# Kernel optimization log

Measured on AMD Instinct MI355X. Metric: run time of the kernel, lower is better.

The kernel has to match this reference:

```python
import jax, jax.numpy as jnp
import numpy as np

B, C2D, C3D, NC = 8, 256, 512, 128
H = W = 64
T = H3 = W3 = 16


def setup_inputs() -> dict:
    key = jax.random.key(0)
    ks = jax.random.split(key, 12)
    s = 0.02
    return {
        "features_2d": jax.random.normal(ks[0], (B, C2D, H, W), jnp.float32),
        "features_3d": jax.random.normal(ks[1], (B, C3D, T, H3, W3), jnp.float32),
        "Wq": jax.random.normal(ks[2], (NC, C2D), jnp.float32) * s,
        "bq": jax.random.normal(ks[3], (NC,), jnp.float32) * s,
        "Wk": jax.random.normal(ks[4], (NC, C3D), jnp.float32) * s,
        "bk": jax.random.normal(ks[5], (NC,), jnp.float32) * s,
        "Wv": jax.random.normal(ks[6], (NC, C3D), jnp.float32) * s,
        "bv": jax.random.normal(ks[7], (NC,), jnp.float32) * s,
        "Wo": jax.random.normal(ks[8], (C2D, NC), jnp.float32) * s,
        "bo": jax.random.normal(ks[9], (C2D,), jnp.float32) * s,
        "Wps": jax.random.normal(ks[10], (C2D, C2D, 3, 3), jnp.float32) * s,
        "bps": jax.random.normal(ks[11], (C2D,), jnp.float32) * s,
    }


def reference(features_2d, features_3d, Wq, bq, Wk, bk, Wv, bv, Wo, bo, Wps, bps):
    # 1x1 conv Q over 2D features: [B, NC, H*W] -> [B, N2d, NC]
    Q = jnp.einsum("bchw,oc->bohw", features_2d, Wq) + bq[None, :, None, None]
    Q = Q.reshape(B, NC, H * W).transpose(0, 2, 1)          # [B, N2d, NC]
    # 1x1 conv K/V over 3D features (no pooling: H3 <= max_height_3d)
    K = jnp.einsum("bcthw,oc->bothw", features_3d, Wk) + bk[None, :, None, None, None]
    V = jnp.einsum("bcthw,oc->bothw", features_3d, Wv) + bv[None, :, None, None, None]
    K = K.reshape(B, NC, T * H3 * W3)                        # [B, NC, N3d]
    V = V.reshape(B, NC, T * H3 * W3).transpose(0, 2, 1)     # [B, N3d, NC]
    # full non-local attention (no 1/sqrt(d) scaling, matching the torch code)
    att = jnp.einsum("bnc,bcm->bnm", Q, K)                   # [B, N2d, N3d]
    att = jax.nn.softmax(att, axis=-1)
    out = jnp.einsum("bnm,bmc->bnc", att, V)                 # [B, N2d, NC]
    out = out.transpose(0, 2, 1).reshape(B, NC, H, W)
    # 1x1 output conv back to channels_2d
    out = jnp.einsum("bchw,oc->bohw", out, Wo) + bo[None, :, None, None]
    # residual add + 3x3 post-sum conv
    x = features_2d + out
    y = jax.lax.conv_general_dilated(
        x, Wps, window_strides=(1, 1), padding="SAME",
        dimension_numbers=("NCHW", "OIHW", "NCHW"))
    return y + bps[None, :, None, None]
```

## Files before the change

kernel.cpp:

```cpp
#include <hip/hip_runtime.h>
#include <cstdint>

#define NB  8
#define C2  256
#define C3  512
#define NCH 128
#define NN2 4096
#define NN3 4096

using f4 = float4;
typedef float f32x16 __attribute__((ext_vector_type(16)));
typedef __bf16 bf16x8 __attribute__((ext_vector_type(8)));

union FragU {
    uint4    q;
    uint32_t u[4];
    bf16x8   v;
};

__device__ __forceinline__ unsigned short f2bf(float f) {
    uint32_t u = __float_as_uint(f);
    u += 0x7fffu + ((u >> 16) & 1u);
    return (unsigned short)(u >> 16);
}
__device__ __forceinline__ float bf2f(unsigned short h) {
    return __uint_as_float(((uint32_t)h) << 16);
}
__device__ __forceinline__ uint32_t pkbf(float lo, float hi) {
    union { __bf16 h[2]; uint32_t u; } t;
    t.h[0] = (__bf16)lo;
    t.h[1] = (__bf16)hi;
    return t.u;
}
__device__ __forceinline__ void fma4(float* acc, float a, const f4 w) {
    acc[0] = fmaf(a, w.x, acc[0]);
    acc[1] = fmaf(a, w.y, acc[1]);
    acc[2] = fmaf(a, w.z, acc[2]);
    acc[3] = fmaf(a, w.w, acc[3]);
}

__global__ __launch_bounds__(256) void wprep(const float* __restrict__ Wps,
                                             unsigned short* __restrict__ Wb) {
    int idx = blockIdx.x * 256 + threadIdx.x;
    int t = idx >> 16;
    int r = idx & 65535;
    int co = r >> 8, ci = r & 255;
    Wb[idx] = f2bf(Wps[((size_t)(co * 256 + ci)) * 9 + t]);
}

__global__ __launch_bounds__(256) void wprep2(const float* __restrict__ Wq,
                                              const float* __restrict__ Wk,
                                              const float* __restrict__ Wv,
                                              unsigned short* __restrict__ Wqb,
                                              unsigned short* __restrict__ Wkb,
                                              unsigned short* __restrict__ Wvb) {
    int idx = blockIdx.x * 256 + threadIdx.x;
    if (idx < 32768)        Wqb[idx]          = f2bf(Wq[idx]);
    else if (idx < 98304)   Wkb[idx - 32768]  = f2bf(Wk[idx - 32768]);
    else                    Wvb[idx - 98304]  = f2bf(Wv[idx - 98304]);
}

__global__ __launch_bounds__(256) void proj_q(const float* __restrict__ f2d,
                                              const unsigned short* __restrict__ Wqb,
                                              const float* __restrict__ bq,
                                              unsigned short* __restrict__ Q) {
    __shared__ __align__(16) unsigned short Xs[2][128 * 40];
    const int tid = threadIdx.x;
    const int b  = blockIdx.x >> 5;
    const int n0 = (blockIdx.x & 31) << 7;
    const int wn = tid >> 6;
    const int lane = tid & 63;
    const int i31 = lane & 31;
    const int h   = lane >> 5;
    const int kp = tid >> 4;
    const int nc = tid & 15;

    f32x16 aQ[4];
#pragma unroll
    for (int cf = 0; cf < 4; cf++)
#pragma unroll
        for (int r = 0; r < 16; r++) aQ[cf][r] = 0.f;

    float xlo[8], xhi[8];
    auto LOADC = [&](int k0) {
        const float* r0 = f2d + ((size_t)b * C2 + k0 + 2 * kp) * NN2 + n0 + nc;
        const float* r1 = r0 + NN2;
#pragma unroll
        for (int i = 0; i < 8; i++) { xlo[i] = r0[16 * i]; xhi[i] = r1[16 * i]; }
    };
    auto WRITEC = [&](int bi) {
        unsigned short* X = Xs[bi];
#pragma unroll
        for (int i = 0; i < 8; i++)
            *(uint32_t*)&X[(nc + 16 * i) * 40 + 2 * kp] = pkbf(xlo[i], xhi[i]);
    };

    LOADC(0); WRITEC(0); __syncthreads();
    int cur = 0;
    for (int c = 0; c < 8; c++) {
        if (c + 1 < 8) LOADC((c + 1) * 32);
        const int k0 = c * 32;
        FragU xf[2];
        xf[0].q = *(const uint4*)&Xs[cur][(wn * 32 + i31) * 40 + h * 8];
        xf[1].q = *(const uint4*)&Xs[cur][(wn * 32 + i31) * 40 + 16 + h * 8];
#pragma unroll
        for (int ks = 0; ks < 2; ks++) {
            const int ko = k0 + ks * 16 + h * 8;
#pragma unroll
            for (int cf = 0; cf < 4; cf++) {
                FragU wq;
                wq.q = *(const uint4*)&Wqb[(size_t)(cf * 32 + i31) * 256 + ko];
                aQ[cf] = __builtin_amdgcn_mfma_f32_32x32x16_bf16(wq.v, xf[ks].v, aQ[cf], 0, 0, 0);
            }
        }
        if (c + 1 < 8) WRITEC(cur ^ 1);
        __syncthreads();
        cur ^= 1;
    }
    const int nQ = n0 + wn * 32 + i31;
    unsigned short* Qrow = Q + ((size_t)b * NN2 + nQ) * NCH;
#pragma unroll
    for (int cf = 0; cf < 4; cf++)
#pragma unroll
        for (int tq = 0; tq < 4; tq++) {
            int c0 = cf * 32 + 8 * tq + 4 * h;
            f4 bb = *(const f4*)(bq + c0);
            ushort4 s;
            s.x = f2bf(aQ[cf][4 * tq + 0] + bb.x);
            s.y = f2bf(aQ[cf][4 * tq + 1] + bb.y);
            s.z = f2bf(aQ[cf][4 * tq + 2] + bb.z);
            s.w = f2bf(aQ[cf][4 * tq + 3] + bb.w);
            *(ushort4*)(Qrow + c0) = s;
        }
}

__global__ __launch_bounds__(256) void proj_kv(const float* __restrict__ f3d,
                                               const unsigned short* __restrict__ Wkb,
                                               const float* __restrict__ bk,
                                               const unsigned short* __restrict__ Wvb,
                                               const float* __restrict__ bv,
                                               unsigned short* __restrict__ K,
                                               unsigned short* __restrict__ Vt) {
    __shared__ __align__(16) unsigned short Xs[2][128 * 40];
    const int tid = threadIdx.x;
    const int b  = blockIdx.x >> 5;
    const int n0 = (blockIdx.x & 31) << 7;
    const int wn = tid >> 6;
    const int lane = tid & 63;
    const int i31 = lane & 31;
    const int h   = lane >> 5;
    const int kp = tid >> 4;
    const int nc = tid & 15;

    f32x16 aK[4], aV[4];
#pragma unroll
    for (int cf = 0; cf < 4; cf++)
#pragma unroll
        for (int r = 0; r < 16; r++) { aK[cf][r] = 0.f; aV[cf][r] = 0.f; }

    float xlo[8], xhi[8];
    auto LOADC = [&](int k0) {
        const float* r0 = f3d + ((size_t)b * C3 + k0 + 2 * kp) * NN3 + n0 + nc;
        const float* r1 = r0 + NN3;
#pragma unroll
        for (int i = 0; i < 8; i++) { xlo[i] = r0[16 * i]; xhi[i] = r1[16 * i]; }
    };
    auto WRITEC = [&](int bi) {
        unsigned short* X = Xs[bi];
#pragma unroll
        for (int i = 0; i < 8; i++)
            *(uint32_t*)&X[(nc + 16 * i) * 40 + 2 * kp] = pkbf(xlo[i], xhi[i]);
    };

    LOADC(0); WRITEC(0); __syncthreads();
    int cur = 0;
    for (int c = 0; c < 16; c++) {
        if (c + 1 < 16) LOADC((c + 1) * 32);
        const int k0 = c * 32;
        FragU xf[2];
        xf[0].q = *(const uint4*)&Xs[cur][(wn * 32 + i31) * 40 + h * 8];
        xf[1].q = *(const uint4*)&Xs[cur][(wn * 32 + i31) * 40 + 16 + h * 8];
#pragma unroll
        for (int ks = 0; ks < 2; ks++) {
            const int ko = k0 + ks * 16 + h * 8;
#pragma unroll
            for (int cf = 0; cf < 4; cf++) {
                FragU wk, wv;
                wk.q = *(const uint4*)&Wkb[(size_t)(cf * 32 + i31) * 512 + ko];
                wv.q = *(const uint4*)&Wvb[(size_t)(cf * 32 + i31) * 512 + ko];
                aK[cf] = __builtin_amdgcn_mfma_f32_32x32x16_bf16(wk.v, xf[ks].v, aK[cf], 0, 0, 0);
                aV[cf] = __builtin_amdgcn_mfma_f32_32x32x16_bf16(xf[ks].v, wv.v, aV[cf], 0, 0, 0);
            }
        }
        if (c + 1 < 16) WRITEC(cur ^ 1);
        __syncthreads();
        cur ^= 1;
    }
    const int nK = n0 + wn * 32 + i31;
    unsigned short* Krow = K + ((size_t)b * NN3 + nK) * NCH;
#pragma unroll
    for (int cf = 0; cf < 4; cf++)
#pragma unroll
        for (int tq = 0; tq < 4; tq++) {
            int c0 = cf * 32 + 8 * tq + 4 * h;
            f4 bb = *(const f4*)(bk + c0);
            ushort4 s;
            s.x = f2bf(aK[cf][4 * tq + 0] + bb.x);
            s.y = f2bf(aK[cf][4 * tq + 1] + bb.y);
            s.z = f2bf(aK[cf][4 * tq + 2] + bb.z);
            s.w = f2bf(aK[cf][4 * tq + 3] + bb.w);
            *(ushort4*)(Krow + c0) = s;
        }
#pragma unroll
    for (int cf = 0; cf < 4; cf++) {
        const int cV = cf * 32 + i31;
        const float bvv = bv[cV];
        unsigned short* Vrow = Vt + ((size_t)b * NCH + cV) * NN3;
#pragma unroll
        for (int tq = 0; tq < 4; tq++) {
            int nq = n0 + wn * 32 + 8 * tq + 4 * h;
            ushort4 s;
            s.x = f2bf(aV[cf][4 * tq + 0] + bvv);
            s.y = f2bf(aV[cf][4 * tq + 1] + bvv);
            s.z = f2bf(aV[cf][4 * tq + 2] + bvv);
            s.w = f2bf(aV[cf][4 * tq + 3] + bvv);
            *(ushort4*)(Vrow + nq) = s;
        }
    }
}

__global__ __launch_bounds__(256) void attn(const unsigned short* __restrict__ Qg,
                                            const unsigned short* __restrict__ Kg,
                                            const unsigned short* __restrict__ Vtg,
                                            unsigned short* __restrict__ AO) {
    __shared__ __align__(16) unsigned short smem[32768];
    const int tid = threadIdx.x;
    const int b  = blockIdx.x >> 6;
    const int qc = blockIdx.x & 63;
    const int wid = tid >> 6;
    const int lane = tid & 63;
    const int i31 = lane & 31;
    const int h   = lane >> 5;
    const int p    = wid >> 1;
    const int tid2 = tid & 127;
    const int q0w  = qc * 64 + (wid & 1) * 32;
    const int kbase = p * 2048;
    unsigned short* Ksp = smem + p * 16384;
    unsigned short* Vsp = smem + p * 16384 + 8192;

    uint4 qf[8];
    const unsigned short* Qrow = Qg + ((size_t)b * NN2 + q0w + i31) * NCH;
#pragma unroll
    for (int dc = 0; dc < 8; dc++) qf[dc] = *(const uint4*)(Qrow + dc * 16 + h * 8);

    f32x16 o[4];
#pragma unroll
    for (int cf = 0; cf < 4; cf++)
#pragma unroll
        for (int r = 0; r < 16; r++) o[cf][r] = 0.f;
    float m_run = -3.0e38f, l_run = 0.f;

    const unsigned short* Kb = Kg  + (size_t)b * NN3 * NCH;
    const unsigned short* Vb = Vtg + (size_t)b * NCH * NN3;

    uint4 kst[4], vst[4];
#pragma unroll
    for (int j = 0; j < 4; j++) {
        int idx = tid2 + 128 * j;
        int key = idx >> 4, g = idx & 15;
        kst[j] = *(const uint4*)(Kb + (size_t)(kbase + key) * NCH + g * 8);
        int c = idx >> 2, gm = idx & 3;
        vst[j] = *(const uint4*)(Vb + (size_t)c * NN3 + kbase + gm * 8);
    }
#pragma unroll
    for (int j = 0; j < 4; j++) {
        int idx = tid2 + 128 * j;
        int key = idx >> 4, g = idx & 15;
        *(uint4*)(&Ksp[key * 128 + ((g ^ (key & 7)) * 8)]) = kst[j];
        int c = idx >> 2, gm = idx & 3;
        *(uint4*)(&Vsp[c * 32 + ((gm ^ (c & 3)) * 8)]) = vst[j];
    }
    __syncthreads();

    int buf = 0;
    for (int t = 0; t < 64; t++) {
        const bool more = (t + 1 < 64);
        if (more) {
            const int m0n = kbase + (t + 1) * 32;
#pragma unroll
            for (int j = 0; j < 4; j++) {
                int idx = tid2 + 128 * j;
                int key = idx >> 4, g = idx & 15;
                kst[j] = *(const uint4*)(Kb + (size_t)(m0n + key) * NCH + g * 8);
                int c = idx >> 2, gm = idx & 3;
                vst[j] = *(const uint4*)(Vb + (size_t)c * NN3 + m0n + gm * 8);
            }
        }
        f32x16 sacc;
#pragma unroll
        for (int r = 0; r < 16; r++) sacc[r] = 0.f;
        __builtin_amdgcn_s_setprio(1);
#pragma unroll
        for (int dc = 0; dc < 8; dc++) {
            FragU bq; bq.q = qf[dc];
            FragU ak;
            ak.q = *(const uint4*)(&Ksp[buf * 4096 + i31 * 128 + (((2 * dc + h) ^ (i31 & 7)) * 8)]);
            sacc = __builtin_amdgcn_mfma_f32_32x32x16_bf16(ak.v, bq.v, sacc, 0, 0, 0);
        }
        __builtin_amdgcn_s_setprio(0);
        float tmax = -3.0e38f;
#pragma unroll
        for (int r = 0; r < 16; r++) tmax = fmaxf(tmax, sacc[r]);
        tmax = fmaxf(tmax, __shfl_xor(tmax, 32, 64));
        if (__any(tmax > m_run)) {
            float newm = fmaxf(m_run, tmax);
            float scale = __expf(m_run - newm);
            m_run = newm;
            l_run *= scale;
#pragma unroll
            for (int reg = 0; reg < 16; reg++) {
                int qrow = (reg & 3) + 8 * (reg >> 2) + 4 * h;
                float sc = __shfl(scale, qrow, 64);
#pragma unroll
                for (int cf = 0; cf < 4; cf++) o[cf][reg] *= sc;
            }
        }
        float psum = 0.f;
#pragma unroll
        for (int r = 0; r < 16; r++) {
            float e = __expf(sacc[r] - m_run);
            sacc[r] = e;
            psum += e;
        }
        psum += __shfl_xor(psum, 32, 64);
        l_run += psum;
        uint32_t pk[8];
#pragma unroll
        for (int j = 0; j < 8; j++) pk[j] = pkbf(sacc[2 * j], sacc[2 * j + 1]);
        __builtin_amdgcn_s_setprio(1);
#pragma unroll
        for (int kc = 0; kc < 2; kc++) {
            uint32_t own_lo  = pk[4 * kc + 0];
            uint32_t own_lo2 = pk[4 * kc + 1];
            uint32_t own_hi  = pk[4 * kc + 2];
            uint32_t own_hi2 = pk[4 * kc + 3];
            uint32_t send1 = h ? own_lo  : own_hi;
            uint32_t send2 = h ? own_lo2 : own_hi2;
            uint32_t recv1 = (uint32_t)__shfl_xor((int)send1, 32, 64);
            uint32_t recv2 = (uint32_t)__shfl_xor((int)send2, 32, 64);
            FragU pa;
            pa.u[0] = h ? recv1 : own_lo;
            pa.u[1] = h ? recv2 : own_lo2;
            pa.u[2] = h ? own_hi  : recv1;
            pa.u[3] = h ? own_hi2 : recv2;
#pragma unroll
            for (int cf = 0; cf < 4; cf++) {
                FragU vbf;
                vbf.q = *(const uint4*)(&Vsp[buf * 4096 + (cf * 32 + i31) * 32 + (((2 * kc + h) ^ (i31 & 3)) * 8)]);
                o[cf] = __builtin_amdgcn_mfma_f32_32x32x16_bf16(pa.v, vbf.v, o[cf], 0, 0, 0);
            }
        }
        __builtin_amdgcn_s_setprio(0);
        if (more) {
#pragma unroll
            for (int j = 0; j < 4; j++) {
                int idx = tid2 + 128 * j;
                int key = idx >> 4, g = idx & 15;
                *(uint4*)(&Ksp[(buf ^ 1) * 4096 + key * 128 + ((g ^ (key & 7)) * 8)]) = kst[j];
                int c = idx >> 2, gm = idx & 3;
                *(uint4*)(&Vsp[(buf ^ 1) * 4096 + c * 32 + ((gm ^ (c & 3)) * 8)]) = vst[j];
            }
        }
        __syncthreads();
        buf ^= 1;
    }
    float* mo = (float*)smem;
    const int s = wid & 1;
    if (wid >= 2) {
        float* mos = mo + s * 4224;
#pragma unroll
        for (int cf = 0; cf < 4; cf++)
#pragma unroll
            for (int reg = 0; reg < 16; reg++) {
                int qrow = (reg & 3) + 8 * (reg >> 2) + 4 * h;
                mos[qrow * 132 + cf * 32 + i31] = o[cf][reg];
            }
        float* ml = mo + 8448;
        if (h == 0) { ml[s * 64 + i31] = m_run; ml[s * 64 + 32 + i31] = l_run; }
    }
    __syncthreads();
    if (wid < 2) {
        float* mos = mo + s * 4224;
        float* ml  = mo + 8448;
        float m2 = ml[s * 64 + i31];
        float l2 = ml[s * 64 + 32 + i31];
        float M  = fmaxf(m_run, m2);
        float a0 = __expf(m_run - M);
        float a2 = __expf(m2 - M);
        float inv = 1.0f / (a0 * l_run + a2 * l2);
#pragma unroll
        for (int reg = 0; reg < 16; reg++) {
            int qrow = (reg & 3) + 8 * (reg >> 2) + 4 * h;
            float a0q = __shfl(a0, qrow, 64);
            float a2q = __shfl(a2, qrow, 64);
            float ivq = __shfl(inv, qrow, 64);
            unsigned short* row = AO + ((size_t)b * NN2 + q0w + qrow) * NCH;
#pragma unroll
            for (int cf = 0; cf < 4; cf++) {
                float val = (a0q * o[cf][reg] + a2q * mos[qrow * 132 + cf * 32 + i31]) * ivq;
                row[cf * 32 + i31] = f2bf(val);
            }
        }
    }
}

__global__ __launch_bounds__(256) void outproj(const unsigned short* __restrict__ AO,
                                               const float* __restrict__ Wo,
                                               const float* __restrict__ bo,
                                               const float* __restrict__ f2d,
                                               unsigned short* __restrict__ Xn) {
    __shared__ __align__(16) float smem[2176 + 4224];
    float* Wt = smem;
    float* At = smem + 2176;
    const int tid = threadIdx.x;
    const int b = blockIdx.x >> 7;
    const int r = blockIdx.x & 127;
    const int co0 = (r >> 5) << 6;
    const int n0  = (r & 31) << 7;
    const int tx = tid & 15, ty = tid >> 4;
    float acc[4][2][4];
#pragma unroll
    for (int i = 0; i < 4; i++)
#pragma unroll
        for (int v = 0; v < 2; v++)
#pragma unroll
            for (int u = 0; u < 4; u++) acc[i][v][u] = 0.f;
    for (int c0 = 0; c0 < NCH; c0 += 32) {
#pragma unroll
        for (int i = 0; i < 2; i++) {
            int cidx = tid + 256 * i;
            int cr = cidx >> 3, koff = (cidx & 7) << 2;
            f4 w = *(const f4*)(Wo + (co0 + cr) * NCH + c0 + koff);
            Wt[(koff + 0) * 68 + cr] = w.x;
            Wt[(koff + 1) * 68 + cr] = w.y;
            Wt[(koff + 2) * 68 + cr] = w.z;
            Wt[(koff + 3) * 68 + cr] = w.w;
        }
#pragma unroll
        for (int i = 0; i < 4; i++) {
            int cidx = tid + 256 * i;
            int nn = cidx >> 3, koff = (cidx & 7) << 2;
            ushort4 a4 = *(const ushort4*)(AO + ((size_t)b * NN2 + n0 + nn) * NCH + c0 + koff);
            At[(koff + 0) * 132 + nn] = bf2f(a4.x);
            At[(koff + 1) * 132 + nn] = bf2f(a4.y);
            At[(koff + 2) * 132 + nn] = bf2f(a4.z);
            At[(koff + 3) * 132 + nn] = bf2f(a4.w);
        }
        __syncthreads();
#pragma unroll 8
        for (int kk = 0; kk < 32; kk++) {
            f4 a4 = *(const f4*)(Wt + kk * 68 + 4 * ty);
            f4 x0 = *(const f4*)(At + kk * 132 + 4 * tx);
            f4 x1 = *(const f4*)(At + kk * 132 + 4 * tx + 64);
            float av[4] = {a4.x, a4.y, a4.z, a4.w};
#pragma unroll
            for (int i = 0; i < 4; i++) { fma4(acc[i][0], av[i], x0); fma4(acc[i][1], av[i], x1); }
        }
        __syncthreads();
    }
    unsigned short* tb = (unsigned short*)smem;
#pragma unroll
    for (int i = 0; i < 4; i++) {
        int co = co0 + 4 * ty + i;
        float bias = bo[co];
        const size_t rowb = ((size_t)b * C2 + co) * NN2 + n0;
#pragma unroll
        for (int v = 0; v < 2; v++) {
            size_t pidx = rowb + 4 * tx + 64 * v;
            f4 f = *(const f4*)(f2d + pidx);
            int nl = 4 * tx + 64 * v;
            tb[(nl + 0) * 72 + 4 * ty + i] = f2bf(acc[i][v][0] + bias + f.x);
            tb[(nl + 1) * 72 + 4 * ty + i] = f2bf(acc[i][v][1] + bias + f.y);
            tb[(nl + 2) * 72 + 4 * ty + i] = f2bf(acc[i][v][2] + bias + f.z);
            tb[(nl + 3) * 72 + 4 * ty + i] = f2bf(acc[i][v][3] + bias + f.w);
        }
    }
    __syncthreads();
#pragma unroll
    for (int k = 0; k < 4; k++) {
        int unit = tid + 256 * k;
        int nl = unit >> 3, cc = unit & 7;
        uint4 d = *(const uint4*)(tb + nl * 72 + cc * 8);
        *(uint4*)(Xn + ((size_t)b * NN2 + n0 + nl) * C2 + co0 + cc * 8) = d;
    }
}

__global__ __launch_bounds__(256) void conv3x3(const unsigned short* __restrict__ Xn,
                                               const unsigned short* __restrict__ Wb,
                                               const float* __restrict__ bps,
                                               float* __restrict__ Y) {
    __shared__ __align__(16) unsigned short Xs[680 * 8];
    const int tid = threadIdx.x;
    const int b  = blockIdx.x >> 6;
    const int r  = blockIdx.x & 63;
    const int ct = r >> 4;
    const int pt = r & 15;
    const int px0 = (pt & 1) << 5;
    const int py0 = (pt >> 1) << 3;
    const int w    = tid >> 6;
    const int lane = tid & 63;
    const int i31  = lane & 31;
    const int h    = lane >> 5;
    const int co0  = ct << 6;

    f32x16 acc[2][2];
#pragma unroll
    for (int ch = 0; ch < 2; ch++)
#pragma unroll
        for (int pf = 0; pf < 2; pf++)
#pragma unroll
            for (int q = 0; q < 16; q++) acc[ch][pf][q] = 0.f;

    const unsigned short* Xb = Xn + (size_t)b * NN2 * C2;

    uint4 sreg[3];
    int su[3], sy[3], sx[3], sh[3];
#pragma unroll
    for (int k = 0; k < 3; k++) {
        int u = tid + 256 * k;
        su[k] = (u < 680);
        int pix = u >> 1;
        sy[k] = pix / 34;
        sx[k] = pix - sy[k] * 34;
        sh[k] = u & 1;
    }

    auto stage_load = [&](int ci0) {
#pragma unroll
        for (int k = 0; k < 3; k++) {
            uint4 z = {0, 0, 0, 0};
            if (su[k]) {
                int gy = py0 - 1 + sy[k];
                int gx = px0 - 1 + sx[k];
                if ((unsigned)gy < 64u && (unsigned)gx < 64u)
                    z = *(const uint4*)(Xb + ((size_t)(gy * 64 + gx)) * C2 + ci0 + 8 * sh[k]);
            }
            sreg[k] = z;
        }
    };
    auto stage_write = [&]() {
#pragma unroll
        for (int k = 0; k < 3; k++) {
            if (su[k]) {
                int slot = (sy[k] * 2 + sh[k]) * 34 + sx[k];
                *(uint4*)(&Xs[slot * 8]) = sreg[k];
            }
        }
    };

    stage_load(0);
    stage_write();
    __syncthreads();

    for (int c = 0; c < 16; c++) {
        if (c + 1 < 16) stage_load((c + 1) * 16);
        const int ci0 = c * 16;
#pragma unroll
        for (int t = 0; t < 9; t++) {
            const int dy = t / 3, dx = t - dy * 3;
            FragU a0, a1;
            a0.q = *(const uint4*)(Wb + ((size_t)(t * 256 + co0 + i31)) * 256 + ci0 + 8 * h);
            a1.q = *(const uint4*)(Wb + ((size_t)(t * 256 + co0 + 32 + i31)) * 256 + ci0 + 8 * h);
#pragma unroll
            for (int pf = 0; pf < 2; pf++) {
                const int yl = 2 * w + pf;
                FragU bx;
                bx.q = *(const uint4*)(&Xs[(((yl + dy) * 2 + h) * 34 + i31 + dx) * 8]);
                acc[0][pf] = __builtin_amdgcn_mfma_f32_32x32x16_bf16(a0.v, bx.v, acc[0][pf], 0, 0, 0);
                acc[1][pf] = __builtin_amdgcn_mfma_f32_32x32x16_bf16(a1.v, bx.v, acc[1][pf], 0, 0, 0);
            }
        }
        __syncthreads();
        if (c + 1 < 16) stage_write();
        __syncthreads();
    }

#pragma unroll
    for (int ch = 0; ch < 2; ch++)
#pragma unroll
        for (int pf = 0; pf < 2; pf++) {
            const int y = py0 + 2 * w + pf;
            const int x = px0 + i31;
#pragma unroll
            for (int q = 0; q < 16; q++) {
                int co = co0 + ch * 32 + (q & 3) + 8 * (q >> 2) + 4 * h;
                Y[(((size_t)b * C2 + co) * 64 + y) * 64 + x] = acc[ch][pf][q] + bps[co];
            }
        }
}

extern "C" void kernel_launch(void* const* d_in, const int* in_sizes, int n_in,
                              void* d_out, int out_size, void* d_ws, size_t ws_size,
                              hipStream_t stream) {
    const float* f2d = (const float*)d_in[0];
    const float* f3d = (const float*)d_in[1];
    const float* Wq  = (const float*)d_in[2];
    const float* bq  = (const float*)d_in[3];
    const float* Wk  = (const float*)d_in[4];
    const float* bk  = (const float*)d_in[5];
    const float* Wv  = (const float*)d_in[6];
    const float* bv  = (const float*)d_in[7];
    const float* Wo  = (const float*)d_in[8];
    const float* bo  = (const float*)d_in[9];
    const float* Wps = (const float*)d_in[10];
    const float* bps = (const float*)d_in[11];
    float* Y = (float*)d_out;

    unsigned short* Qb  = (unsigned short*)d_ws;
    unsigned short* Kb  = Qb + 4194304;
    unsigned short* Vtb = Kb + 4194304;
    unsigned short* AOb = Vtb + 4194304;
    unsigned short* Xnb = AOb + 4194304;
    unsigned short* Wbb = Xnb + 8388608;
    unsigned short* Wqb = Wbb + 589824;
    unsigned short* Wkb = Wqb + 32768;
    unsigned short* Wvb = Wkb + 65536;

    dim3 blk(256);
    wprep   <<<dim3(2304), blk, 0, stream>>>(Wps, Wbb);
    wprep2  <<<dim3(640),  blk, 0, stream>>>(Wq, Wk, Wv, Wqb, Wkb, Wvb);
    proj_q  <<<dim3(256),  blk, 0, stream>>>(f2d, Wqb, bq, Qb);
    proj_kv <<<dim3(256),  blk, 0, stream>>>(f3d, Wkb, bk, Wvb, bv, Kb, Vtb);
    attn    <<<dim3(512),  blk, 0, stream>>>(Qb, Kb, Vtb, AOb);
    outproj <<<dim3(1024), blk, 0, stream>>>(AOb, Wo, bo, f2d, Xnb);
    conv3x3 <<<dim3(512),  blk, 0, stream>>>(Xnb, Wbb, bps, Y);
}
```

Measured before the change: 612.5 us.

## Split attention into single-wave split-K partial kernel plus separate merge kernel

Replaces the four-wave attention block with one-wave blocks. Each block handles 32 queries over half the keys and writes a normalized partial output plus its running max and sum. A new elementwise kernel then merges the two halves into the attention output. This removes the block-wide barriers, the LDS-based in-block merge and the XOR swizzle, and uses padded LDS rows instead of the swizzle. The cost is that K/V tiles are no longer shared between two waves, an extra kernel launch, and a bf16 round trip for the partials. The max/sum buffer is placed past the existing weight workspace, so it depends on the workspace being large enough.

```diff
diff --git a/kernel.cpp b/kernel.cpp
--- a/kernel.cpp
+++ b/kernel.cpp
@@ -99,13 +99,12 @@
     int cur = 0;
     for (int c = 0; c < 8; c++) {
         if (c + 1 < 8) LOADC((c + 1) * 32);
-        const int k0 = c * 32;
         FragU xf[2];
         xf[0].q = *(const uint4*)&Xs[cur][(wn * 32 + i31) * 40 + h * 8];
         xf[1].q = *(const uint4*)&Xs[cur][(wn * 32 + i31) * 40 + 16 + h * 8];
 #pragma unroll
         for (int ks = 0; ks < 2; ks++) {
-            const int ko = k0 + ks * 16 + h * 8;
+            const int ko = c * 32 + ks * 16 + h * 8;
 #pragma unroll
             for (int cf = 0; cf < 4; cf++) {
                 FragU wq;
@@ -176,13 +175,12 @@
     int cur = 0;
     for (int c = 0; c < 16; c++) {
         if (c + 1 < 16) LOADC((c + 1) * 32);
-        const int k0 = c * 32;
         FragU xf[2];
         xf[0].q = *(const uint4*)&Xs[cur][(wn * 32 + i31) * 40 + h * 8];
         xf[1].q = *(const uint4*)&Xs[cur][(wn * 32 + i31) * 40 + 16 + h * 8];
 #pragma unroll
         for (int ks = 0; ks < 2; ks++) {
-            const int ko = k0 + ks * 16 + h * 8;
+            const int ko = c * 32 + ks * 16 + h * 8;
 #pragma unroll
             for (int cf = 0; cf < 4; cf++) {
                 FragU wk, wv;
@@ -229,27 +227,25 @@
     }
 }
 
-__global__ __launch_bounds__(256) void attn(const unsigned short* __restrict__ Qg,
-                                            const unsigned short* __restrict__ Kg,
-                                            const unsigned short* __restrict__ Vtg,
-                                            unsigned short* __restrict__ AO) {
-    __shared__ __align__(16) unsigned short smem[32768];
+__global__ __launch_bounds__(64, 2) void attn_part(const unsigned short* __restrict__ Qg,
+                                                   const unsigned short* __restrict__ Kg,
+                                                   const unsigned short* __restrict__ Vtg,
+                                                   unsigned short* __restrict__ Op,
+                                                   float* __restrict__ Ml) {
+    __shared__ __align__(16) unsigned short Ks[32 * 136];
+    __shared__ __align__(16) unsigned short Vs[128 * 40];
     const int tid = threadIdx.x;
-    const int b  = blockIdx.x >> 6;
-    const int qc = blockIdx.x & 63;
-    const int wid = tid >> 6;
-    const int lane = tid & 63;
-    const int i31 = lane & 31;
-    const int h   = lane >> 5;
-    const int p    = wid >> 1;
-    const int tid2 = tid & 127;
-    const int q0w  = qc * 64 + (wid & 1) * 32;
+    const int b  = blockIdx.x >> 8;
+    const int r  = blockIdx.x & 255;
+    const int qc = r >> 1;
+    const int p  = r & 1;
+    const int i31 = tid & 31;
+    const int h   = tid >> 5;
+    const int q0 = qc * 32;
     const int kbase = p * 2048;
-    unsigned short* Ksp = smem + p * 16384;
-    unsigned short* Vsp = smem + p * 16384 + 8192;
 
     uint4 qf[8];
-    const unsigned short* Qrow = Qg + ((size_t)b * NN2 + q0w + i31) * NCH;
+    const unsigned short* Qrow = Qg + ((size_t)b * NN2 + q0 + i31) * NCH;
 #pragma unroll
     for (int dc = 0; dc < 8; dc++) qf[dc] = *(const uint4*)(Qrow + dc * 16 + h * 8);
 
@@ -257,60 +253,55 @@
 #pragma unroll
     for (int cf = 0; cf < 4; cf++)
 #pragma unroll
-        for (int r = 0; r < 16; r++) o[cf][r] = 0.f;
+        for (int r2 = 0; r2 < 16; r2++) o[cf][r2] = 0.f;
     float m_run = -3.0e38f, l_run = 0.f;
 
     const unsigned short* Kb = Kg  + (size_t)b * NN3 * NCH;
     const unsigned short* Vb = Vtg + (size_t)b * NCH * NN3;
 
-    uint4 kst[4], vst[4];
-#pragma unroll
-    for (int j = 0; j < 4; j++) {
-        int idx = tid2 + 128 * j;
-        int key = idx >> 4, g = idx & 15;
-        kst[j] = *(const uint4*)(Kb + (size_t)(kbase + key) * NCH + g * 8);
-        int c = idx >> 2, gm = idx & 3;
-        vst[j] = *(const uint4*)(Vb + (size_t)c * NN3 + kbase + gm * 8);
-    }
-#pragma unroll
-    for (int j = 0; j < 4; j++) {
-        int idx = tid2 + 128 * j;
-        int key = idx >> 4, g = idx & 15;
-        *(uint4*)(&Ksp[key * 128 + ((g ^ (key & 7)) * 8)]) = kst[j];
-        int c = idx >> 2, gm = idx & 3;
-        *(uint4*)(&Vsp[c * 32 + ((gm ^ (c & 3)) * 8)]) = vst[j];
-    }
-    __syncthreads();
-
-    int buf = 0;
+    uint4 kst[8], vst[8];
+    auto LOADKV = [&](int m0) {
+#pragma unroll
+        for (int j = 0; j < 8; j++) {
+            int u = tid + 64 * j;
+            int key = u >> 4, g = u & 15;
+            kst[j] = *(const uint4*)(Kb + (size_t)(kbase + m0 + key) * NCH + g * 8);
+            int c = u >> 2, gm = u & 3;
+            vst[j] = *(const uint4*)(Vb + (size_t)c * NN3 + kbase + m0 + gm * 8);
+        }
+    };
+    auto WRITEKV = [&]() {
+#pragma unroll
+        for (int j = 0; j < 8; j++) {
+            int u = tid + 64 * j;
+            int key = u >> 4, g = u & 15;
+            *(uint4*)(&Ks[key * 136 + g * 8]) = kst[j];
+            int c = u >> 2, gm = u & 3;
+            *(uint4*)(&Vs[c * 40 + gm * 8]) = vst[j];
+        }
+    };
+
+    LOADKV(0);
+    WRITEKV();
+
     for (int t = 0; t < 64; t++) {
         const bool more = (t + 1 < 64);
-        if (more) {
-            const int m0n = kbase + (t + 1) * 32;
-#pragma unroll
-            for (int j = 0; j < 4; j++) {
-                int idx = tid2 + 128 * j;
-                int key = idx >> 4, g = idx & 15;
-                kst[j] = *(const uint4*)(Kb + (size_t)(m0n + key) * NCH + g * 8);
-                int c = idx >> 2, gm = idx & 3;
-                vst[j] = *(const uint4*)(Vb + (size_t)c * NN3 + m0n + gm * 8);
-            }
-        }
+        if (more) LOADKV((t + 1) * 32);
         f32x16 sacc;
 #pragma unroll
-        for (int r = 0; r < 16; r++) sacc[r] = 0.f;
+        for (int r2 = 0; r2 < 16; r2++) sacc[r2] = 0.f;
         __builtin_amdgcn_s_setprio(1);
 #pragma unroll
         for (int dc = 0; dc < 8; dc++) {
             FragU bq; bq.q = qf[dc];
             FragU ak;
-            ak.q = *(const uint4*)(&Ksp[buf * 4096 + i31 * 128 + (((2 * dc + h) ^ (i31 & 7)) * 8)]);
+            ak.q = *(const uint4*)(&Ks[i31 * 136 + (2 * dc + h) * 8]);
             sacc = __builtin_amdgcn_mfma_f32_32x32x16_bf16(ak.v, bq.v, sacc, 0, 0, 0);
         }
         __builtin_amdgcn_s_setprio(0);
         float tmax = -3.0e38f;
 #pragma unroll
-        for (int r = 0; r < 16; r++) tmax = fmaxf(tmax, sacc[r]);
+        for (int r2 = 0; r2 < 16; r2++) tmax = fmaxf(tmax, sacc[r2]);
         tmax = fmaxf(tmax, __shfl_xor(tmax, 32, 64));
         if (__any(tmax > m_run)) {
             float newm = fmaxf(m_run, tmax);
@@ -327,9 +318,9 @@
         }
         float psum = 0.f;
 #pragma unroll
-        for (int r = 0; r < 16; r++) {
-            float e = __expf(sacc[r] - m_run);
-            sacc[r] = e;
+        for (int r2 = 0; r2 < 16; r2++) {
+            float e = __expf(sacc[r2] - m_run);
+            sacc[r2] = e;
             psum += e;
         }
         psum += __shfl_xor(psum, 32, 64);
@@ -356,62 +347,60 @@
 #pragma unroll
             for (int cf = 0; cf < 4; cf++) {
                 FragU vbf;
-                vbf.q = *(const uint4*)(&Vsp[buf * 4096 + (cf * 32 + i31) * 32 + (((2 * kc + h) ^ (i31 & 3)) * 8)]);
+                vbf.q = *(const uint4*)(&Vs[(cf * 32 + i31) * 40 + (2 * kc + h) * 8]);
                 o[cf] = __builtin_amdgcn_mfma_f32_32x32x16_bf16(pa.v, vbf.v, o[cf], 0, 0, 0);
             }
         }
         __builtin_amdgcn_s_setprio(0);
-        if (more) {
-#pragma unroll
-            for (int j = 0; j < 4; j++) {
-                int idx = tid2 + 128 * j;
-                int key = idx >> 4, g = idx & 15;
-                *(uint4*)(&Ksp[(buf ^ 1) * 4096 + key * 128 + ((g ^ (key & 7)) * 8)]) = kst[j];
-                int c = idx >> 2, gm = idx & 3;
-                *(uint4*)(&Vsp[(buf ^ 1) * 4096 + c * 32 + ((gm ^ (c & 3)) * 8)]) = vst[j];
-            }
-        }
-        __syncthreads();
-        buf ^= 1;
-    }
-    float* mo = (float*)smem;
-    const int s = wid & 1;
-    if (wid >= 2) {
-        float* mos = mo + s * 4224;
-#pragma unroll
-        for (int cf = 0; cf < 4; cf++)
-#pragma unroll
-            for (int reg = 0; reg < 16; reg++) {
-                int qrow = (reg & 3) + 8 * (reg >> 2) + 4 * h;
-                mos[qrow * 132 + cf * 32 + i31] = o[cf][reg];
-            }
-        float* ml = mo + 8448;
-        if (h == 0) { ml[s * 64 + i31] = m_run; ml[s * 64 + 32 + i31] = l_run; }
-    }
-    __syncthreads();
-    if (wid < 2) {
-        float* mos = mo + s * 4224;
-        float* ml  = mo + 8448;
-        float m2 = ml[s * 64 + i31];
-        float l2 = ml[s * 64 + 32 + i31];
-        float M  = fmaxf(m_run, m2);
-        float a0 = __expf(m_run - M);
-        float a2 = __expf(m2 - M);
-        float inv = 1.0f / (a0 * l_run + a2 * l2);
-#pragma unroll
-        for (int reg = 0; reg < 16; reg++) {
-            int qrow = (reg & 3) + 8 * (reg >> 2) + 4 * h;
-            float a0q = __shfl(a0, qrow, 64);
-            float a2q = __shfl(a2, qrow, 64);
-            float ivq = __shfl(inv, qrow, 64);
-            unsigned short* row = AO + ((size_t)b * NN2 + q0w + qrow) * NCH;
-#pragma unroll
-            for (int cf = 0; cf < 4; cf++) {
-                float val = (a0q * o[cf][reg] + a2q * mos[qrow * 132 + cf * 32 + i31]) * ivq;
-                row[cf * 32 + i31] = f2bf(val);
-            }
-        }
-    }
+        if (more) WRITEKV();
+    }
+    float inv = 1.0f / l_run;
+#pragma unroll
+    for (int reg = 0; reg < 16; reg++) {
+        int qrow = (reg & 3) + 8 * (reg >> 2) + 4 * h;
+        float iv = __shfl(inv, qrow, 64);
+        unsigned short* row = Op + (((size_t)p * NB + b) * NN2 + q0 + qrow) * NCH;
+#pragma unroll
+        for (int cf = 0; cf < 4; cf++) row[cf * 32 + i31] = f2bf(o[cf][reg] * iv);
+    }
+    if (h == 0) {
+        int bn = b * NN2 + q0 + i31;
+        Ml[p * 32768 + bn]         = m_run;
+        Ml[65536 + p * 32768 + bn] = l_run;
+    }
+}
+
+__global__ __launch_bounds__(256) void attn_merge(const unsigned short* __restrict__ Op,
+                                                  const float* __restrict__ Ml,
+                                                  unsigned short* __restrict__ AO) {
+    int idx = blockIdx.x * 256 + threadIdx.x;
+    int bn = idx >> 4;
+    int cu = (idx & 15) * 8;
+    float m0 = Ml[bn],         l0 = Ml[65536 + bn];
+    float m1 = Ml[32768 + bn], l1 = Ml[98304 + bn];
+    float M  = fmaxf(m0, m1);
+    float w0 = __expf(m0 - M) * l0;
+    float w1 = __expf(m1 - M) * l1;
+    float inv = 1.0f / (w0 + w1);
+    float a0 = w0 * inv, a1 = w1 * inv;
+    const unsigned short* p0 = Op + (size_t)bn * NCH + cu;
+    const unsigned short* p1 = Op + ((size_t)NB * NN2 + bn) * NCH + cu;
+    ushort4 x0a = *(const ushort4*)p0;
+    ushort4 x0b = *(const ushort4*)(p0 + 4);
+    ushort4 x1a = *(const ushort4*)p1;
+    ushort4 x1b = *(const ushort4*)(p1 + 4);
+    ushort4 ra, rb;
+    ra.x = f2bf(a0 * bf2f(x0a.x) + a1 * bf2f(x1a.x));
+    ra.y = f2bf(a0 * bf2f(x0a.y) + a1 * bf2f(x1a.y));
+    ra.z = f2bf(a0 * bf2f(x0a.z) + a1 * bf2f(x1a.z));
+    ra.w = f2bf(a0 * bf2f(x0a.w) + a1 * bf2f(x1a.w));
+    rb.x = f2bf(a0 * bf2f(x0b.x) + a1 * bf2f(x1b.x));
+    rb.y = f2bf(a0 * bf2f(x0b.y) + a1 * bf2f(x1b.y));
+    rb.z = f2bf(a0 * bf2f(x0b.z) + a1 * bf2f(x1b.z));
+    rb.w = f2bf(a0 * bf2f(x0b.w) + a1 * bf2f(x1b.w));
+    unsigned short* out = AO + (size_t)bn * NCH + cu;
+    *(ushort4*)out = ra;
+    *(ushort4*)(out + 4) = rb;
 }
 
 __global__ __launch_bounds__(256) void outproj(const unsigned short* __restrict__ AO,
@@ -625,13 +614,15 @@
     unsigned short* Wqb = Wbb + 589824;
     unsigned short* Wkb = Wqb + 32768;
     unsigned short* Wvb = Wkb + 65536;
+    float* Ml = (float*)(Wvb + 65536);
 
     dim3 blk(256);
-    wprep   <<<dim3(2304), blk, 0, stream>>>(Wps, Wbb);
-    wprep2  <<<dim3(640),  blk, 0, stream>>>(Wq, Wk, Wv, Wqb, Wkb, Wvb);
-    proj_q  <<<dim3(256),  blk, 0, stream>>>(f2d, Wqb, bq, Qb);
-    proj_kv <<<dim3(256),  blk, 0, stream>>>(f3d, Wkb, bk, Wvb, bv, Kb, Vtb);
-    attn    <<<dim3(512),  blk, 0, stream>>>(Qb, Kb, Vtb, AOb);
-    outproj <<<dim3(1024), blk, 0, stream>>>(AOb, Wo, bo, f2d, Xnb);
-    conv3x3 <<<dim3(512),  blk, 0, stream>>>(Xnb, Wbb, bps, Y);
-}
+    wprep     <<<dim3(2304), blk, 0, stream>>>(Wps, Wbb);
+    wprep2    <<<dim3(640),  blk, 0, stream>>>(Wq, Wk, Wv, Wqb, Wkb, Wvb);
+    proj_q    <<<dim3(256),  blk, 0, stream>>>(f2d, Wqb, bq, Qb);
+    proj_kv   <<<dim3(256),  blk, 0, stream>>>(f3d, Wkb, bk, Wvb, bv, Kb, Vtb);
+    attn_part <<<dim3(2048), dim3(64), 0, stream>>>(Qb, Kb, Vtb, Xnb, Ml);
+    attn_merge<<<dim3(2048), blk, 0, stream>>>(Xnb, Ml, AOb);
+    outproj   <<<dim3(1024), blk, 0, stream>>>(AOb, Wo, bo, f2d, Xnb);
+    conv3x3   <<<dim3(512),  blk, 0, stream>>>(Xnb, Wbb, bps, Y);
+}
```

Measured after the change: 867.2 us. 1.42x slower.
